# Kernel tuning notes

Hardware: AMD Instinct MI355X
Metric: run time of the kernel (lower is better)

The kernel has to match this reference:

```python
import jax, jax.numpy as jnp
import numpy as np

MD = 4            # max_displacement
DP = 1            # dilation_patch
PATCH = 2 * MD + 1  # 9
# kernel_size=1, stride=1, padding=0, dilation=1 -> oH=H, oW=W


def setup_inputs() -> dict:
    key = jax.random.key(0)
    k1, k2 = jax.random.split(key)
    N, C, H, W = 8, 256, 128, 128
    input1 = jax.random.normal(k1, (N, C, H, W), dtype=jnp.float32)
    input2 = jax.random.normal(k2, (N, C, H, W), dtype=jnp.float32)
    return {"input1": input1, "input2": input2}


def _correlation(input1, input2):
    # out[n, py, px, y, x] = sum_c input1[n,c,y,x] * input2[n,c, y+(py-MD)*DP, x+(px-MD)*DP]
    # with zero padding for out-of-bounds input2 positions (mmcv semantics, no
    # normalization by channel count).
    N, C, H, W = input1.shape
    pad = MD * DP
    x2 = jnp.pad(input2, ((0, 0), (0, 0), (pad, pad), (pad, pad)))
    rows = []
    for py in range(PATCH):  # small fixed displacement grid (9x9)
        cols = []
        for px in range(PATCH):
            sh, sw = py * DP, px * DP
            x2s = x2[:, :, sh:sh + H, sw:sw + W]  # shifted input2, [N,C,H,W]
            cols.append(jnp.einsum('nchw,nchw->nhw', input1, x2s))
        rows.append(jnp.stack(cols, axis=1))  # [N, PATCH, H, W]
    return jnp.stack(rows, axis=1)  # [N, PATCH, PATCH, H, W]


def reference(input1, input2):
    return _correlation(input1, input2)
```

## Files before the change

### kernel.cpp

```cpp
#include <hip/hip_runtime.h>
#include <hip/hip_bf16.h>
#include <limits.h>

typedef __attribute__((ext_vector_type(8))) short short8v;
typedef __attribute__((ext_vector_type(4))) short short4v;
typedef __attribute__((ext_vector_type(4))) float f32x4;

#define H_  128
#define W_  128
#define C_  256
#define HW_ 16384

#define MFMA32(a, b, c) __builtin_amdgcn_mfma_f32_16x16x32_bf16(a, b, c, 0, 0, 0)

__device__ __forceinline__ short bf16b(float f) {
    unsigned u = __float_as_uint(f);
    u += 0x7fffu + ((u >> 16) & 1u);
    return (short)(u >> 16);
}

__global__ __launch_bounds__(512, 2)
void corr_kernel(const float* __restrict__ in1, const float* __restrict__ in2,
                 float* __restrict__ out)
{
    __shared__ short lds2[2][24 * 4 * 32 * 8];
    __shared__ float ldso[9 * 257];

    const int tid  = threadIdx.x;
    const int lane = tid & 63;
    const int wid  = tid >> 6;
    const int m    = lane & 15;
    const int g    = lane >> 4;

    int bid = blockIdx.x;
    int swz = (bid & 7) * 64 + (bid >> 3);
    int n   = swz >> 6;
    int h0  = ((swz >> 3) & 7) << 4;
    int w0  = (swz & 7) << 4;

    const float* in1n = in1 + (size_t)n * (C_ * HW_);
    const float* in2n = in2 + (size_t)n * (C_ * HW_);

    int lwoff[9]; int gofs[9];
#pragma unroll
    for (int s = 0; s < 9; ++s) {
        int u    = tid + s * 512;
        int q    = u % 6;
        int rest = u / 6;
        int i    = rest & 7;
        int rj   = rest >> 3;
        int j    = rj & 3;
        int r    = rj >> 2;
        int row  = h0 - 4 + r;
        int col0 = w0 - 4 + 4 * q;
        bool inb = ((unsigned)row < 128u) && ((unsigned)col0 < 125u);
        gofs[s]  = inb ? ((j * 8 + i) * HW_ + row * W_ + col0) : INT_MIN;
        lwoff[s] = ((r * 4 + j) * 32 + 4 * q) * 8 + i;
    }
    const int abase = (8 * g) * HW_ + (h0 + 2 * wid) * W_ + (w0 + m);

    {
        short8v z = (short8v)0;
        short8v* zp = (short8v*)&lds2[0][0];
#pragma unroll
        for (int i = 0; i < 12; ++i) zp[tid + i * 512] = z;
    }
    __syncthreads();
    __builtin_amdgcn_sched_barrier(0);

    f32x4 acc[2][9][2];
#pragma unroll
    for (int a = 0; a < 2; ++a)
#pragma unroll
        for (int d = 0; d < 9; ++d)
#pragma unroll
            for (int t = 0; t < 2; ++t)
                acc[a][d][t] = (f32x4){0.f, 0.f, 0.f, 0.f};

    {
        f32x4 sv[9];
#pragma unroll
        for (int s = 0; s < 9; ++s) {
            f32x4 v = (f32x4){0.f, 0.f, 0.f, 0.f};
            if (gofs[s] != INT_MIN) v = *(const f32x4*)(in2n + gofs[s]);
            sv[s] = v;
        }
#pragma unroll
        for (int s = 0; s < 9; ++s) {
            short* p = &lds2[0][lwoff[s]];
#pragma unroll
            for (int d = 0; d < 4; ++d) p[8 * d] = bf16b(sv[s][d]);
        }
    }

#pragma unroll 1
    for (int t = 0; t < 8; ++t) {
        __syncthreads();
        __builtin_amdgcn_sched_barrier(0);
        const int rb = t & 1;

        float af[2][8];
#pragma unroll
        for (int rs = 0; rs < 2; ++rs)
#pragma unroll
            for (int i = 0; i < 8; ++i)
                af[rs][i] = in1n[abase + (32 * t + i) * HW_ + rs * W_];

        f32x4 sv[9];
        if (t < 7) {
            const int koff = (t + 1) * 32 * HW_;
#pragma unroll
            for (int s = 0; s < 9; ++s) {
                f32x4 v = (f32x4){0.f, 0.f, 0.f, 0.f};
                if (gofs[s] != INT_MIN) v = *(const f32x4*)(in2n + gofs[s] + koff);
                sv[s] = v;
            }
        }

        short8v a8[2];
#pragma unroll
        for (int rs = 0; rs < 2; ++rs)
#pragma unroll
            for (int i = 0; i < 8; ++i) a8[rs][i] = bf16b(af[rs][i]);

        const short* lb = &lds2[rb][0];
#pragma unroll
        for (int rr = 0; rr < 10; ++rr) {
            int ro = (((2 * wid + rr) * 4 + g) * 32) * 8;
            short8v b0 = *(const short8v*)&lb[ro + m * 8];
            short8v b1 = *(const short8v*)&lb[ro + (16 + m) * 8];
            if (rr <= 8) {
                acc[0][rr][0] = MFMA32(a8[0], b0, acc[0][rr][0]);
                acc[0][rr][1] = MFMA32(a8[0], b1, acc[0][rr][1]);
            }
            if (rr >= 1) {
                acc[1][rr - 1][0] = MFMA32(a8[1], b0, acc[1][rr - 1][0]);
                acc[1][rr - 1][1] = MFMA32(a8[1], b1, acc[1][rr - 1][1]);
            }
        }

        if (t < 7) {
#pragma unroll
            for (int s = 0; s < 9; ++s) {
                short* p = &lds2[rb ^ 1][lwoff[s]];
#pragma unroll
                for (int d = 0; d < 4; ++d) p[8 * d] = bf16b(sv[s][d]);
            }
        }
    }

    const size_t outb = (size_t)n * 81 * HW_;
#pragma unroll
    for (int dy = 0; dy < 9; ++dy) {
        __syncthreads();
        __builtin_amdgcn_sched_barrier(0);
#pragma unroll
        for (int rs = 0; rs < 2; ++rs) {
            int hl = 2 * wid + rs;
#pragma unroll
            for (int nt = 0; nt < 2; ++nt) {
#pragma unroll
                for (int i = 0; i < 4; ++i) {
                    int mm = 4 * g + i;
                    int dx = nt * 16 + m - mm;
                    if (dx >= 0 && dx < 9)
                        ldso[dx * 257 + hl * 16 + mm] = acc[rs][dy][nt][i];
                }
            }
        }
        __syncthreads();
        __builtin_amdgcn_sched_barrier(0);
#pragma unroll
        for (int e = 0; e < 5; ++e) {
            int t = tid + e * 512;
            if (t < 2304) {
                int dx  = t >> 8;
                int rem = t & 255;
                out[outb + (size_t)(dy * 9 + dx) * HW_ +
                    (size_t)(h0 + (rem >> 4)) * W_ + (w0 + (rem & 15))] = ldso[dx * 257 + rem];
            }
        }
    }
}

extern "C" void kernel_launch(void* const* d_in, const int* in_sizes, int n_in,
                              void* d_out, int out_size, void* d_ws, size_t ws_size,
                              hipStream_t stream) {
    const float* in1 = (const float*)d_in[0];
    const float* in2 = (const float*)d_in[1];
    float* out = (float*)d_out;
    corr_kernel<<<dim3(512), dim3(512), 0, stream>>>(in1, in2, out);
}
```

Measured before the change: 98.69 us.

## Triple-buffer LDS and prefetch two K-chunks ahead with packed bf16 stores

Moves from double to triple buffering of the shifted input2 tile in LDS. Global loads now run two chunks ahead, and LDS writes for the next chunk happen before the MFMA loop instead of after it. It also packs channel pairs into 32-bit bf16 stores to halve LDS store instructions, prefetches input1 one chunk ahead in registers, and aliases the output staging buffer onto the same shared memory. The goal is to hide global load latency behind the MFMA work. The cost is more LDS (144KB) and more registers held across iterations, which may limit occupancy below the requested 2 blocks per CU.

Measured after the change: 98.24 us. About the same (-0.4%).

```diff
diff --git a/kernel.cpp b/kernel.cpp
--- a/kernel.cpp
+++ b/kernel.cpp
@@ -1,9 +1,7 @@
 #include <hip/hip_runtime.h>
-#include <hip/hip_bf16.h>
 #include <limits.h>
 
 typedef __attribute__((ext_vector_type(8))) short short8v;
-typedef __attribute__((ext_vector_type(4))) short short4v;
 typedef __attribute__((ext_vector_type(4))) float f32x4;
 
 #define H_  128
@@ -18,13 +16,22 @@
     u += 0x7fffu + ((u >> 16) & 1u);
     return (short)(u >> 16);
 }
+__device__ __forceinline__ unsigned bf16pk(float lo, float hi) {
+    unsigned ul = __float_as_uint(lo);
+    ul += 0x7fffu + ((ul >> 16) & 1u);
+    unsigned uh = __float_as_uint(hi);
+    uh += 0x7fffu + ((uh >> 16) & 1u);
+    return (ul >> 16) | (uh & 0xffff0000u);
+}
 
 __global__ __launch_bounds__(512, 2)
 void corr_kernel(const float* __restrict__ in1, const float* __restrict__ in2,
                  float* __restrict__ out)
 {
-    __shared__ short lds2[2][24 * 4 * 32 * 8];
-    __shared__ float ldso[9 * 257];
+    __shared__ __attribute__((aligned(16))) unsigned char smem[3 * 49152];
+    short*    lds  = (short*)smem;
+    unsigned* ldsI = (unsigned*)smem;
+    float*    ldso = (float*)smem;
 
     const int tid  = threadIdx.x;
     const int lane = tid & 63;
@@ -41,89 +48,119 @@
     const float* in1n = in1 + (size_t)n * (C_ * HW_);
     const float* in2n = in2 + (size_t)n * (C_ * HW_);
 
-    int lwoff[9]; int gofs[9];
-#pragma unroll
-    for (int s = 0; s < 9; ++s) {
+    int lwdw[5]; int gof0[5];
+#pragma unroll
+    for (int s = 0; s < 5; ++s) {
         int u    = tid + s * 512;
+        bool act = (u < 2304);
         int q    = u % 6;
         int rest = u / 6;
-        int i    = rest & 7;
-        int rj   = rest >> 3;
-        int j    = rj & 3;
-        int r    = rj >> 2;
+        int kp   = rest & 15;
+        int r    = rest >> 4;
         int row  = h0 - 4 + r;
         int col0 = w0 - 4 + 4 * q;
-        bool inb = ((unsigned)row < 128u) && ((unsigned)col0 < 125u);
-        gofs[s]  = inb ? ((j * 8 + i) * HW_ + row * W_ + col0) : INT_MIN;
-        lwoff[s] = ((r * 4 + j) * 32 + 4 * q) * 8 + i;
+        bool inb = act && ((unsigned)row < 128u) && ((unsigned)col0 < 125u);
+        int  cc  = 8 * (kp >> 2) + 2 * (kp & 3);
+        gof0[s]  = inb ? (cc * HW_ + row * W_ + col0) : INT_MIN;
+        lwdw[s]  = ((r * 4 + (kp >> 2)) * 32 + 4 * q) * 4 + (kp & 3);
     }
     const int abase = (8 * g) * HW_ + (h0 + 2 * wid) * W_ + (w0 + m);
 
     {
         short8v z = (short8v)0;
-        short8v* zp = (short8v*)&lds2[0][0];
-#pragma unroll
-        for (int i = 0; i < 12; ++i) zp[tid + i * 512] = z;
-    }
+        short8v* zp = (short8v*)lds;
+#pragma unroll
+        for (int i = 0; i < 18; ++i) zp[tid + i * 512] = z;
+    }
+
+    f32x4 acc[2][9][2];
+#pragma unroll
+    for (int a = 0; a < 2; ++a)
+#pragma unroll
+        for (int d = 0; d < 9; ++d)
+#pragma unroll
+            for (int t = 0; t < 2; ++t)
+                acc[a][d][t] = (f32x4){0.f, 0.f, 0.f, 0.f};
+
     __syncthreads();
     __builtin_amdgcn_sched_barrier(0);
 
-    f32x4 acc[2][9][2];
-#pragma unroll
-    for (int a = 0; a < 2; ++a)
-#pragma unroll
-        for (int d = 0; d < 9; ++d)
-#pragma unroll
-            for (int t = 0; t < 2; ++t)
-                acc[a][d][t] = (f32x4){0.f, 0.f, 0.f, 0.f};
-
-    {
-        f32x4 sv[9];
-#pragma unroll
-        for (int s = 0; s < 9; ++s) {
+    f32x4 sf[5][2];
+    float afn[2][8];
+
+#pragma unroll
+    for (int s = 0; s < 5; ++s)
+#pragma unroll
+        for (int e = 0; e < 2; ++e) {
             f32x4 v = (f32x4){0.f, 0.f, 0.f, 0.f};
-            if (gofs[s] != INT_MIN) v = *(const f32x4*)(in2n + gofs[s]);
-            sv[s] = v;
-        }
-#pragma unroll
-        for (int s = 0; s < 9; ++s) {
-            short* p = &lds2[0][lwoff[s]];
-#pragma unroll
-            for (int d = 0; d < 4; ++d) p[8 * d] = bf16b(sv[s][d]);
-        }
-    }
+            if (gof0[s] != INT_MIN) v = *(const f32x4*)(in2n + gof0[s] + e * HW_);
+            sf[s][e] = v;
+        }
+#pragma unroll
+    for (int s = 0; s < 5; ++s)
+        if (tid + s * 512 < 2304) {
+#pragma unroll
+            for (int d = 0; d < 4; ++d)
+                ldsI[lwdw[s] + 4 * d] = bf16pk(sf[s][0][d], sf[s][1][d]);
+        }
+#pragma unroll
+    for (int s = 0; s < 5; ++s)
+#pragma unroll
+        for (int e = 0; e < 2; ++e) {
+            f32x4 v = (f32x4){0.f, 0.f, 0.f, 0.f};
+            if (gof0[s] != INT_MIN) v = *(const f32x4*)(in2n + gof0[s] + e * HW_ + 32 * HW_);
+            sf[s][e] = v;
+        }
+#pragma unroll
+    for (int rs = 0; rs < 2; ++rs)
+#pragma unroll
+        for (int i = 0; i < 8; ++i)
+            afn[rs][i] = in1n[abase + i * HW_ + rs * W_];
 
 #pragma unroll 1
     for (int t = 0; t < 8; ++t) {
         __syncthreads();
         __builtin_amdgcn_sched_barrier(0);
-        const int rb = t & 1;
-
-        float af[2][8];
+        const int bcur  = t % 3;
+        const int wnext = (t + 1) % 3;
+
+        short8v a8[2];
 #pragma unroll
         for (int rs = 0; rs < 2; ++rs)
 #pragma unroll
-            for (int i = 0; i < 8; ++i)
-                af[rs][i] = in1n[abase + (32 * t + i) * HW_ + rs * W_];
-
-        f32x4 sv[9];
+            for (int i = 0; i < 8; ++i) a8[rs][i] = bf16b(afn[rs][i]);
+
         if (t < 7) {
-            const int koff = (t + 1) * 32 * HW_;
-#pragma unroll
-            for (int s = 0; s < 9; ++s) {
-                f32x4 v = (f32x4){0.f, 0.f, 0.f, 0.f};
-                if (gofs[s] != INT_MIN) v = *(const f32x4*)(in2n + gofs[s] + koff);
-                sv[s] = v;
-            }
-        }
-
-        short8v a8[2];
-#pragma unroll
-        for (int rs = 0; rs < 2; ++rs)
-#pragma unroll
-            for (int i = 0; i < 8; ++i) a8[rs][i] = bf16b(af[rs][i]);
-
-        const short* lb = &lds2[rb][0];
+            unsigned* wp = ldsI + wnext * 12288;
+#pragma unroll
+            for (int s = 0; s < 5; ++s)
+                if (tid + s * 512 < 2304) {
+#pragma unroll
+                    for (int d = 0; d < 4; ++d)
+                        wp[lwdw[s] + 4 * d] = bf16pk(sf[s][0][d], sf[s][1][d]);
+                }
+        }
+        if (t < 6) {
+            const int koff = (t + 2) * 32 * HW_;
+#pragma unroll
+            for (int s = 0; s < 5; ++s)
+#pragma unroll
+                for (int e = 0; e < 2; ++e) {
+                    f32x4 v = (f32x4){0.f, 0.f, 0.f, 0.f};
+                    if (gof0[s] != INT_MIN) v = *(const f32x4*)(in2n + gof0[s] + e * HW_ + koff);
+                    sf[s][e] = v;
+                }
+        }
+        if (t < 7) {
+            const int akoff = (t + 1) * 32 * HW_;
+#pragma unroll
+            for (int rs = 0; rs < 2; ++rs)
+#pragma unroll
+                for (int i = 0; i < 8; ++i)
+                    afn[rs][i] = in1n[abase + (akoff + i * HW_) + rs * W_];
+        }
+
+        const short* lb = lds + bcur * 24576;
 #pragma unroll
         for (int rr = 0; rr < 10; ++rr) {
             int ro = (((2 * wid + rr) * 4 + g) * 32) * 8;
@@ -138,15 +175,6 @@
                 acc[1][rr - 1][1] = MFMA32(a8[1], b1, acc[1][rr - 1][1]);
             }
         }
-
-        if (t < 7) {
-#pragma unroll
-            for (int s = 0; s < 9; ++s) {
-                short* p = &lds2[rb ^ 1][lwoff[s]];
-#pragma unroll
-                for (int d = 0; d < 4; ++d) p[8 * d] = bf16b(sv[s][d]);
-            }
-        }
     }
 
     const size_t outb = (size_t)n * 81 * HW_;
```
